# Performance work log

Hardware: AMD Instinct MI355X
Metric: run time of the kernel (lower is better)

The kernel has to match this reference:

```python
import jax, jax.numpy as jnp
import numpy as np

N_NODES = 50000
N_EDGES = 800000
IN_DIM = 128
HID = 128
NUM_CLASSES = 2


def setup_inputs() -> dict:
    key = jax.random.key(0)
    ks = jax.random.split(key, 16)
    inp = {
        "adj_row": jax.random.randint(ks[0], (N_EDGES,), 0, N_NODES),
        "adj_col": jax.random.randint(ks[1], (N_EDGES,), 0, N_NODES),
        "adj_vals": jax.random.uniform(ks[2], (N_EDGES,), dtype=jnp.float32),
        "input_feature": jax.random.normal(ks[3], (N_NODES, IN_DIM), dtype=jnp.float32),
        "graph_indicator": jax.random.randint(ks[4], (N_NODES,), 0, 64),
        # GCN layer params (kaiming-uniform-ish init; zeros bias like the torch module)
        "W1": jax.random.uniform(ks[5], (IN_DIM, HID), jnp.float32, -1, 1) * np.sqrt(6.0 / IN_DIM),
        "b1": jnp.zeros((HID,), jnp.float32),
        "W2": jax.random.uniform(ks[6], (HID, HID), jnp.float32, -1, 1) * np.sqrt(6.0 / HID),
        "b2": jnp.zeros((HID,), jnp.float32),
        "W3": jax.random.uniform(ks[7], (HID, HID), jnp.float32, -1, 1) * np.sqrt(6.0 / HID),
        "b3": jnp.zeros((HID,), jnp.float32),
        # fc params (torch.nn.Linear default init range)
        "fcW1": jax.random.uniform(ks[8], (3 * HID, HID), jnp.float32, -1, 1) / np.sqrt(3 * HID),
        "fcb1": jax.random.uniform(ks[9], (HID,), jnp.float32, -1, 1) / np.sqrt(3 * HID),
        "fcW2": jax.random.uniform(ks[10], (HID, HID // 2), jnp.float32, -1, 1) / np.sqrt(HID),
        "fcb2": jax.random.uniform(ks[11], (HID // 2,), jnp.float32, -1, 1) / np.sqrt(HID),
        "fcW3": jax.random.uniform(ks[12], (HID // 2, NUM_CLASSES), jnp.float32, -1, 1) / np.sqrt(HID // 2),
        "fcb3": jax.random.uniform(ks[13], (NUM_CLASSES,), jnp.float32, -1, 1) / np.sqrt(HID // 2),
    }
    return inp


def _gcn_layer(row, col, vals, x, W, b, n_nodes):
    # support = X @ W  -> dense GEMM
    support = x @ W
    # sparse.mm(A, support): out[i] = sum_{e: row[e]=i} vals[e] * support[col[e]]
    msgs = support[col] * vals[:, None]  # [E, D] gather + scale
    agg = jax.ops.segment_sum(msgs, row, num_segments=n_nodes)
    return agg + b


def reference(adj_row, adj_col, adj_vals, input_feature, graph_indicator,
              W1, b1, W2, b2, W3, b3, fcW1, fcb1, fcW2, fcb2, fcW3, fcb3):
    n = input_feature.shape[0]
    g1 = jax.nn.relu(_gcn_layer(adj_row, adj_col, adj_vals, input_feature, W1, b1, n))
    g2 = jax.nn.relu(_gcn_layer(adj_row, adj_col, adj_vals, g1, W2, b2, n))
    g3 = jax.nn.relu(_gcn_layer(adj_row, adj_col, adj_vals, g2, W3, b3, n))
    feat = jnp.concatenate([g1, g2, g3], axis=1)  # [N, 3*HID]
    h = jax.nn.relu(feat @ fcW1 + fcb1)
    h = jax.nn.relu(h @ fcW2 + fcb2)
    logits = h @ fcW3 + fcb3
    return logits
```

## Files before the change

kernel.cpp:

```cpp
#include <hip/hip_runtime.h>
#include <hip/hip_bf16.h>

#define N_NODES 50000
#define N_EDGES 800000
#define NBK 391
#define BCAP 2560
#define PADSLACK 896

static inline int cdiv(int a, int b) { return (a + b - 1) / b; }

typedef __attribute__((ext_vector_type(8))) short short8;
typedef __attribute__((ext_vector_type(4))) float f32x4;

__device__ __forceinline__ float b2f(unsigned short u) {
    union { unsigned int i; float f; } c;
    c.i = ((unsigned int)u) << 16;
    return c.f;
}
__device__ __forceinline__ unsigned short f2bb(float f) {
    __hip_bfloat16 h = __float2bfloat16(f);
    return *(unsigned short*)&h;
}

__device__ __forceinline__ void pack_one(const float* __restrict__ W,
                                         __hip_bfloat16* __restrict__ out,
                                         int K, int N, int t) {
    int lane = t & 63;
    int kc = (t >> 6) % (K / 32);
    int nt = (t >> 6) / (K / 32);
    int kbase = kc * 32 + (lane >> 4) * 8;
    int col = nt * 16 + (lane & 15);
    __hip_bfloat16* dst = out + (size_t)t * 8;
#pragma unroll
    for (int j = 0; j < 8; ++j)
        dst[j] = __float2bfloat16(W[(size_t)(kbase + j) * N + col]);
}

__global__ __launch_bounds__(256)
void stage1_kernel(const int* __restrict__ row, const int* __restrict__ col,
                   const float* __restrict__ vals, int* __restrict__ bcursor,
                   int2* __restrict__ tmp, int E,
                   const float* __restrict__ x, __hip_bfloat16* __restrict__ support,
                   int M,
                   const float* __restrict__ W1, const float* __restrict__ W2,
                   const float* __restrict__ W3, const float* __restrict__ fcW1,
                   const float* __restrict__ fcW2,
                   __hip_bfloat16* __restrict__ pW2, __hip_bfloat16* __restrict__ pW3,
                   __hip_bfloat16* __restrict__ pfcW1, __hip_bfloat16* __restrict__ pfcW2) {
    __shared__ unsigned short As[64][136];
    __shared__ int hist[NBK];
    __shared__ int base[NBK];
    const int b = blockIdx.x;
    const int tid = threadIdx.x;

    if (b < 196) {
        const int CH = 4096;
        int e0 = b * CH;
        for (int i = tid; i < NBK; i += 256) hist[i] = 0;
        __syncthreads();
        for (int i = tid; i < CH; i += 256) {
            int e = e0 + i;
            if (e < E) atomicAdd(&hist[row[e] >> 7], 1);
        }
        __syncthreads();
        for (int i = tid; i < NBK; i += 256) {
            int c = hist[i];
            base[i] = (c > 0) ? (i * BCAP + atomicAdd(&bcursor[i], c)) : 0;
            hist[i] = 0;
        }
        __syncthreads();
        for (int i = tid; i < CH; i += 256) {
            int e = e0 + i;
            if (e < E) {
                int r = row[e];
                int bk = r >> 7;
                int rk = atomicAdd(&hist[bk], 1);
                tmp[base[bk] + rk] = make_int2(((r & 127) << 16) | col[e],
                                               __float_as_int(vals[e]));
            }
        }
        return;
    }

    if (b < 978) {
        const int wave = tid >> 6;
        const int lane = tid & 63;
        const int ln15 = lane & 15;
        const int quad = lane >> 4;
        const int m0 = (b - 196) * 64;

        short8 bfr[4][2];
#pragma unroll
        for (int kc = 0; kc < 4; ++kc)
#pragma unroll
            for (int h = 0; h < 2; ++h)
#pragma unroll
                for (int j = 0; j < 8; ++j)
                    bfr[kc][h][j] = (short)f2bb(
                        W1[(size_t)(kc * 32 + quad * 8 + j) * 128 + (wave * 2 + h) * 16 + ln15]);

#pragma unroll
        for (int i = 0; i < 4; ++i) {
            int idx = tid + i * 256;
            int r = idx >> 4;
            int c8 = (idx & 15) * 8;
            uint4 pk = {0, 0, 0, 0};
            if (m0 + r < M) {
                const float* src = &x[(size_t)(m0 + r) * 128 + c8];
                float4 a = *(const float4*)src;
                float4 bq = *(const float4*)(src + 4);
                pk.x = f2bb(a.x) | ((unsigned int)f2bb(a.y) << 16);
                pk.y = f2bb(a.z) | ((unsigned int)f2bb(a.w) << 16);
                pk.z = f2bb(bq.x) | ((unsigned int)f2bb(bq.y) << 16);
                pk.w = f2bb(bq.z) | ((unsigned int)f2bb(bq.w) << 16);
            }
            *(uint4*)&As[r][c8] = pk;
        }
        __syncthreads();

        f32x4 acc[4][2];
#pragma unroll
        for (int s = 0; s < 4; ++s)
#pragma unroll
            for (int h = 0; h < 2; ++h) acc[s][h] = (f32x4){0.f, 0.f, 0.f, 0.f};
#pragma unroll
        for (int kc = 0; kc < 4; ++kc) {
            short8 af[4];
#pragma unroll
            for (int s = 0; s < 4; ++s)
                af[s] = *(const short8*)&As[s * 16 + ln15][kc * 32 + quad * 8];
#pragma unroll
            for (int s = 0; s < 4; ++s)
#pragma unroll
                for (int h = 0; h < 2; ++h)
                    acc[s][h] = __builtin_amdgcn_mfma_f32_16x16x32_bf16(
                        af[s], bfr[kc][h], acc[s][h], 0, 0, 0);
        }
#pragma unroll
        for (int s = 0; s < 4; ++s)
#pragma unroll
            for (int h = 0; h < 2; ++h) {
                int cl = (wave * 2 + h) * 16 + ln15;
#pragma unroll
                for (int r = 0; r < 4; ++r) {
                    int rw = m0 + s * 16 + quad * 4 + r;
                    if (rw < M)
                        support[(size_t)rw * 128 + cl] = __float2bfloat16(acc[s][h][r]);
                }
            }
        return;
    }

    int pb = b - 978;
    if (pb < 8)       pack_one(W2,  pW2,  128, 128, pb * 256 + tid);
    else if (pb < 16) pack_one(W3,  pW3,  128, 128, (pb - 8) * 256 + tid);
    else if (pb < 40) pack_one(fcW1, pfcW1, 384, 128, (pb - 16) * 256 + tid);
    else              pack_one(fcW2, pfcW2, 128, 64, (pb - 40) * 256 + tid);
}


__global__ __launch_bounds__(512)
void bscan_kernel(const int* __restrict__ bcursor, int* __restrict__ bbase) {
    __shared__ int s[512];
    int t = threadIdx.x;
    int v = (t < NBK) ? bcursor[t] : 0;
    s[t] = v;
    __syncthreads();
    for (int off = 1; off < 512; off <<= 1) {
        int u = (t >= off) ? s[t - off] : 0;
        __syncthreads();
        s[t] += u;
        __syncthreads();
    }
    if (t < NBK) bbase[t] = s[t] - v;
    if (t == NBK - 1) bbase[NBK] = s[t];
}

__global__ __launch_bounds__(256)
void binB_kernel(const int2* __restrict__ tmp, const int* __restrict__ bcursor,
                 const int* __restrict__ bbase, int* __restrict__ row_ptr,
                 int* __restrict__ row_end, int2* __restrict__ epack, int N) {
    int b = blockIdx.x;
    int r0 = b << 7;
    int nr = N - r0; if (nr > 128) nr = 128;
    __shared__ int cnt[128];
    __shared__ int cur[128];
    __shared__ int rpos[128];
    int t = threadIdx.x;
    if (t < 128) cnt[t] = 0;
    __syncthreads();
    int slab = b * BCAP;
    int send = slab + bcursor[b];
    for (int i = slab + t; i < send; i += 256)
        atomicAdd(&cnt[tmp[i].x >> 16], 1);
    __syncthreads();
    int rcnt = (t < 128) ? cnt[t] : 0;
    int pc = (rcnt + 7) & ~7;
    if (t < 128) cur[t] = pc;
    __syncthreads();
    for (int off = 1; off < 128; off <<= 1) {
        int u = (t >= off && t < 128) ? cur[t - off] : 0;
        __syncthreads();
        if (t < 128) cur[t] += u;
        __syncthreads();
    }
    int obase = bbase[b] + b * PADSLACK;
    if (t < 128) {
        int pos = obase + cur[t] - pc;
        rpos[t] = pos;
        cur[t] = pos;
        if (t < nr) {
            row_ptr[r0 + t] = pos;
            row_end[r0 + t] = pos + pc;
        }
    }
    __syncthreads();
    for (int i = slab + t; i < send; i += 256) {
        int2 v = tmp[i];
        int rl = v.x >> 16;
        int c = v.x & 0xffff;
        int pos = atomicAdd(&cur[rl], 1);
        epack[pos] = make_int2(c, v.y);
    }
    if (t < 128) {
        int pos = rpos[t];
#pragma unroll 1
        for (int i = pos + rcnt; i < pos + pc; ++i)
            epack[i] = make_int2(0, 0);
    }
}

__global__ __launch_bounds__(256, 3)
void mfma_gemm(const __hip_bfloat16* __restrict__ A, int lda,
               const __hip_bfloat16* __restrict__ pW,
               __hip_bfloat16* __restrict__ C, int M) {
    __shared__ unsigned short As[64][136];
    const int tid = threadIdx.x;
    const int wave = tid >> 6;
    const int lane = tid & 63;
    const int ln15 = lane & 15;
    const int quad = lane >> 4;
    const int m0 = blockIdx.x * 64;
    const int ntw = wave * 2;

    f32x4 acc[4][2];
#pragma unroll
    for (int s = 0; s < 4; ++s)
#pragma unroll
        for (int h = 0; h < 2; ++h) acc[s][h] = (f32x4){0.f, 0.f, 0.f, 0.f};

#pragma unroll
    for (int i = 0; i < 4; ++i) {
        int idx = tid + i * 256;
        int r = idx >> 4;
        int c8 = (idx & 15) * 8;
        uint4 v = *(const uint4*)&A[(size_t)(m0 + r) * lda + c8];
        *(uint4*)&As[r][c8] = v;
    }
    __syncthreads();
#pragma unroll
    for (int kc = 0; kc < 4; ++kc) {
        short8 af[4];
#pragma unroll
        for (int s = 0; s < 4; ++s)
            af[s] = *(const short8*)&As[s * 16 + ln15][kc * 32 + quad * 8];
        short8 bf[2];
#pragma unroll
        for (int h = 0; h < 2; ++h)
            bf[h] = *(const short8*)&pW[((size_t)((ntw + h) * 4 + kc) * 64 + lane) * 8];
#pragma unroll
        for (int s = 0; s < 4; ++s)
#pragma unroll
            for (int h = 0; h < 2; ++h)
                acc[s][h] = __builtin_amdgcn_mfma_f32_16x16x32_bf16(
                    af[s], bf[h], acc[s][h], 0, 0, 0);
    }

#pragma unroll
    for (int s = 0; s < 4; ++s)
#pragma unroll
        for (int h = 0; h < 2; ++h) {
            int cl = (ntw + h) * 16 + ln15;
#pragma unroll
            for (int r = 0; r < 4; ++r) {
                int rw = m0 + s * 16 + quad * 4 + r;
                if (rw < M)
                    C[(size_t)rw * 128 + cl] = __float2bfloat16(acc[s][h][r]);
            }
        }
}

__global__ __launch_bounds__(256)
void spmm_kernel(const int* __restrict__ row_ptr, const int* __restrict__ row_end,
                 const int2* __restrict__ epack,
                 const __hip_bfloat16* __restrict__ support,
                 const float* __restrict__ bias, __hip_bfloat16* __restrict__ out,
                 int ldo, int n) {
    int wv = threadIdx.x >> 6;
    int l = threadIdx.x & 63;
    int node = blockIdx.x * 4 + wv;
    if (node >= n) return;
    const long long* ep = (const long long*)epack;
    int p = row_ptr[node], end = row_end[node];
    float ax = 0.f, ay = 0.f;
    long long v[8];
    ushort2 u[8];
    bool have = false;
    if (p < end) {
#pragma unroll
        for (int j = 0; j < 8; ++j) v[j] = ep[p + j];
#pragma unroll
        for (int j = 0; j < 8; ++j)
            u[j] = *(const ushort2*)&support[(size_t)(unsigned int)(v[j] & 0xffffffffu) * 128 + l * 2];
        p += 8;
        have = true;
    }
    while (p < end) {
        long long v2[8];
        ushort2 u2[8];
#pragma unroll
        for (int j = 0; j < 8; ++j) v2[j] = ep[p + j];
#pragma unroll
        for (int j = 0; j < 8; ++j)
            u2[j] = *(const ushort2*)&support[(size_t)(unsigned int)(v2[j] & 0xffffffffu) * 128 + l * 2];
#pragma unroll
        for (int j = 0; j < 8; ++j) {
            float f = __int_as_float((int)(v[j] >> 32));
            ax += f * b2f(u[j].x);
            ay += f * b2f(u[j].y);
        }
#pragma unroll
        for (int j = 0; j < 8; ++j) { v[j] = v2[j]; u[j] = u2[j]; }
        p += 8;
    }
    if (have) {
#pragma unroll
        for (int j = 0; j < 8; ++j) {
            float f = __int_as_float((int)(v[j] >> 32));
            ax += f * b2f(u[j].x);
            ay += f * b2f(u[j].y);
        }
    }
    unsigned int packed = (unsigned int)f2bb(fmaxf(ax + bias[l * 2 + 0], 0.f))
                        | ((unsigned int)f2bb(fmaxf(ay + bias[l * 2 + 1], 0.f)) << 16);
    __builtin_nontemporal_store(packed, (unsigned int*)&out[(size_t)node * ldo + l * 2]);
}

__global__ __launch_bounds__(256, 3)
void fc123_kernel(const __hip_bfloat16* __restrict__ featb,
                  const __hip_bfloat16* __restrict__ pfcW1,
                  const float* __restrict__ fcb1,
                  const __hip_bfloat16* __restrict__ pfcW2,
                  const float* __restrict__ fcb2,
                  const float* __restrict__ fcW3, const float* __restrict__ fcb3,
                  float* __restrict__ out, int M) {
    __shared__ unsigned short As[64][136];
    __shared__ float w3s[128];
    __shared__ float b3s[2];
    const int tid = threadIdx.x;
    const int wave = tid >> 6;
    const int lane = tid & 63;
    const int ln15 = lane & 15;
    const int quad = lane >> 4;
    const int m0 = blockIdx.x * 64;
    if (tid < 128) w3s[tid] = fcW3[tid];
    if (tid < 2) b3s[tid] = fcb3[tid];

    f32x4 acc[4][2];
#pragma unroll
    for (int s = 0; s < 4; ++s)
#pragma unroll
        for (int h = 0; h < 2; ++h) acc[s][h] = (f32x4){0.f, 0.f, 0.f, 0.f};
    for (int kb = 0; kb < 3; ++kb) {
#pragma unroll
        for (int i = 0; i < 4; ++i) {
            int idx = tid + i * 256;
            int r = idx >> 4;
            int c8 = (idx & 15) * 8;
            uint4 v = *(const uint4*)&featb[(size_t)(m0 + r) * 384 + kb * 128 + c8];
            *(uint4*)&As[r][c8] = v;
        }
        __syncthreads();
#pragma unroll
        for (int kc = 0; kc < 4; ++kc) {
            short8 af[4];
#pragma unroll
            for (int s = 0; s < 4; ++s)
                af[s] = *(const short8*)&As[s * 16 + ln15][kc * 32 + quad * 8];
            short8 bf[2];
#pragma unroll
            for (int h = 0; h < 2; ++h) {
                int kcg = kb * 4 + kc;
                bf[h] = *(const short8*)&pfcW1[((size_t)((wave * 2 + h) * 12 + kcg) * 64 + lane) * 8];
            }
#pragma unroll
            for (int s = 0; s < 4; ++s)
#pragma unroll
                for (int h = 0; h < 2; ++h)
                    acc[s][h] = __builtin_amdgcn_mfma_f32_16x16x32_bf16(
                        af[s], bf[h], acc[s][h], 0, 0, 0);
        }
        __syncthreads();
    }
#pragma unroll
    for (int s = 0; s < 4; ++s)
#pragma unroll
        for (int h = 0; h < 2; ++h) {
            int col = (wave * 2 + h) * 16 + ln15;
            float bv = fcb1[col];
#pragma unroll
            for (int r = 0; r < 4; ++r) {
                int row = s * 16 + quad * 4 + r;
                As[row][col] = f2bb(fmaxf(acc[s][h][r] + bv, 0.f));
            }
        }
    __syncthreads();

    f32x4 acc2[4];
#pragma unroll
    for (int s = 0; s < 4; ++s) acc2[s] = (f32x4){0.f, 0.f, 0.f, 0.f};
#pragma unroll
    for (int kc = 0; kc < 4; ++kc) {
        short8 af[4];
#pragma unroll
        for (int s = 0; s < 4; ++s)
            af[s] = *(const short8*)&As[s * 16 + ln15][kc * 32 + quad * 8];
        short8 bfw = *(const short8*)&pfcW2[((size_t)(wave * 4 + kc) * 64 + lane) * 8];
#pragma unroll
        for (int s = 0; s < 4; ++s)
            acc2[s] = __builtin_amdgcn_mfma_f32_16x16x32_bf16(af[s], bfw, acc2[s], 0, 0, 0);
    }
    __syncthreads();
    {
        int col2 = wave * 16 + ln15;
        float bv = fcb2[col2];
#pragma unroll
        for (int s = 0; s < 4; ++s)
#pragma unroll
            for (int r = 0; r < 4; ++r) {
                int row = s * 16 + quad * 4 + r;
                As[row][col2] = f2bb(fmaxf(acc2[s][r] + bv, 0.f));
            }
    }
    __syncthreads();

    if (tid < 128) {
        int row = tid >> 1, cls = tid & 1;
        int grow = m0 + row;
        if (grow < M) {
            float a = b3s[cls];
#pragma unroll
            for (int k = 0; k < 64; ++k)
                a += b2f(As[row][k]) * w3s[k * 2 + cls];
            out[(size_t)grow * 2 + cls] = a;
        }
    }
}

extern "C" void kernel_launch(void* const* d_in, const int* in_sizes, int n_in,
                              void* d_out, int out_size, void* d_ws, size_t ws_size,
                              hipStream_t stream) {
    const int*   adj_row  = (const int*)d_in[0];
    const int*   adj_col  = (const int*)d_in[1];
    const float* adj_vals = (const float*)d_in[2];
    const float* x        = (const float*)d_in[3];
    const float* W1   = (const float*)d_in[5];
    const float* b1   = (const float*)d_in[6];
    const float* W2   = (const float*)d_in[7];
    const float* b2   = (const float*)d_in[8];
    const float* W3   = (const float*)d_in[9];
    const float* b3   = (const float*)d_in[10];
    const float* fcW1 = (const float*)d_in[11];
    const float* fcb1 = (const float*)d_in[12];
    const float* fcW2 = (const float*)d_in[13];
    const float* fcb2 = (const float*)d_in[14];
    const float* fcW3 = (const float*)d_in[15];
    const float* fcb3 = (const float*)d_in[16];
    float* out = (float*)d_out;

    const int N = N_NODES, E = N_EDGES;
    const int Mpad = 50048;
    const int EPAD = E + NBK * PADSLACK + 64;

    char* p = (char*)d_ws;
    auto alloc = [&](size_t bytes) {
        char* q = p;
        p += (bytes + 255) & ~(size_t)255;
        return q;
    };
    __hip_bfloat16* featb    = (__hip_bfloat16*)alloc((size_t)Mpad * 384 * 2);
    __hip_bfloat16* supportb = (__hip_bfloat16*)alloc((size_t)Mpad * 128 * 2);
    __hip_bfloat16* pW2   = (__hip_bfloat16*)alloc(16384 * 2);
    __hip_bfloat16* pW3   = (__hip_bfloat16*)alloc(16384 * 2);
    __hip_bfloat16* pfcW1 = (__hip_bfloat16*)alloc(49152 * 2);
    __hip_bfloat16* pfcW2 = (__hip_bfloat16*)alloc(8192 * 2);
    int*   row_ptr   = (int*)alloc((size_t)(N + 1) * 4);
    int*   row_end   = (int*)alloc((size_t)(N + 1) * 4);
    int*   bbase     = (int*)alloc((size_t)(NBK + 1) * 4);
    int*   bcursor   = (int*)alloc((size_t)NBK * 4);
    int2*  epack     = (int2*)alloc((size_t)EPAD * 8);
    int2*  tmp       = (int2*)alloc((size_t)NBK * BCAP * 8);

    hipMemsetAsync(bcursor, 0, (size_t)NBK * 4, stream);
    stage1_kernel<<<1022, 256, 0, stream>>>(adj_row, adj_col, adj_vals, bcursor, tmp, E,
                                            x, supportb, N,
                                            W1, W2, W3, fcW1, fcW2,
                                            pW2, pW3, pfcW1, pfcW2);
    bscan_kernel<<<1, 512, 0, stream>>>(bcursor, bbase);
    binB_kernel<<<NBK, 256, 0, stream>>>(tmp, bcursor, bbase, row_ptr, row_end, epack, N);

    const int gemmGrid = cdiv(N, 64);
    const int spmmGrid = cdiv(N, 4);

    spmm_kernel<<<spmmGrid, 256, 0, stream>>>(row_ptr, row_end, epack, supportb, b1,
                                              featb + 0, 384, N);
    mfma_gemm<<<gemmGrid, 256, 0, stream>>>(featb + 0, 384, pW2, supportb, N);
    spmm_kernel<<<spmmGrid, 256, 0, stream>>>(row_ptr, row_end, epack, supportb, b2,
                                              featb + 128, 384, N);
    mfma_gemm<<<gemmGrid, 256, 0, stream>>>(featb + 128, 384, pW3, supportb, N);
    spmm_kernel<<<spmmGrid, 256, 0, stream>>>(row_ptr, row_end, epack, supportb, b3,
                                              featb + 256, 384, N);

    fc123_kernel<<<gemmGrid, 256, 0, stream>>>(featb, pfcW1, fcb1, pfcW2, fcb2,
                                               fcW3, fcb3, out, N);
}
```

Before: 280.7 us.

## Vectorize SpMM gathers to 16-byte loads and fold bucket scan into binning

The SpMM kernel now splits each wave into four 16-lane groups. Each group gathers a full 256-byte support row with uint4 loads, covering eight edges per iteration, and the partial sums are reduced across groups with shuffles. This replaces eight narrow 4-byte gathers per lane. The separate single-block bucket-scan kernel is removed: each binB block now computes its own prefix sum over bcursor with a block reduction. Row start and end are packed into one int2 array, which adds redundant prefix work per block in exchange for one fewer launch and fewer scattered loads.

```diff
diff --git a/kernel.cpp b/kernel.cpp
--- a/kernel.cpp
+++ b/kernel.cpp
@@ -159,36 +159,26 @@
 }
 
 
-__global__ __launch_bounds__(512)
-void bscan_kernel(const int* __restrict__ bcursor, int* __restrict__ bbase) {
-    __shared__ int s[512];
-    int t = threadIdx.x;
-    int v = (t < NBK) ? bcursor[t] : 0;
-    s[t] = v;
-    __syncthreads();
-    for (int off = 1; off < 512; off <<= 1) {
-        int u = (t >= off) ? s[t - off] : 0;
-        __syncthreads();
-        s[t] += u;
-        __syncthreads();
-    }
-    if (t < NBK) bbase[t] = s[t] - v;
-    if (t == NBK - 1) bbase[NBK] = s[t];
-}
-
 __global__ __launch_bounds__(256)
 void binB_kernel(const int2* __restrict__ tmp, const int* __restrict__ bcursor,
-                 const int* __restrict__ bbase, int* __restrict__ row_ptr,
-                 int* __restrict__ row_end, int2* __restrict__ epack, int N) {
+                 int2* __restrict__ rowrange, int2* __restrict__ epack, int N) {
     int b = blockIdx.x;
     int r0 = b << 7;
     int nr = N - r0; if (nr > 128) nr = 128;
     __shared__ int cnt[128];
     __shared__ int cur[128];
     __shared__ int rpos[128];
+    __shared__ int red[256];
     int t = threadIdx.x;
+    int partial = 0;
+    for (int i = t; i < b; i += 256) partial += bcursor[i];
+    red[t] = partial;
     if (t < 128) cnt[t] = 0;
     __syncthreads();
+    for (int off = 128; off > 0; off >>= 1) {
+        if (t < off) red[t] += red[t + off];
+        __syncthreads();
+    }
     int slab = b * BCAP;
     int send = slab + bcursor[b];
     for (int i = slab + t; i < send; i += 256)
@@ -204,15 +194,12 @@
         if (t < 128) cur[t] += u;
         __syncthreads();
     }
-    int obase = bbase[b] + b * PADSLACK;
+    int obase = red[0] + b * PADSLACK;
     if (t < 128) {
         int pos = obase + cur[t] - pc;
         rpos[t] = pos;
         cur[t] = pos;
-        if (t < nr) {
-            row_ptr[r0 + t] = pos;
-            row_end[r0 + t] = pos + pc;
-        }
+        if (t < nr) rowrange[r0 + t] = make_int2(pos, pos + pc);
     }
     __syncthreads();
     for (int i = slab + t; i < send; i += 256) {
@@ -223,9 +210,10 @@
         epack[pos] = make_int2(c, v.y);
     }
     if (t < 128) {
+        int rc = rcnt;
         int pos = rpos[t];
 #pragma unroll 1
-        for (int i = pos + rcnt; i < pos + pc; ++i)
+        for (int i = pos + rc; i < pos + pc; ++i)
             epack[i] = make_int2(0, 0);
     }
 }
@@ -290,8 +278,20 @@
         }
 }
 
+__device__ __forceinline__ void accum8(float* acc, long long e, uint4 u) {
+    float f = __int_as_float((int)(e >> 32));
+    acc[0] += f * b2f((unsigned short)(u.x & 0xffff));
+    acc[1] += f * b2f((unsigned short)(u.x >> 16));
+    acc[2] += f * b2f((unsigned short)(u.y & 0xffff));
+    acc[3] += f * b2f((unsigned short)(u.y >> 16));
+    acc[4] += f * b2f((unsigned short)(u.z & 0xffff));
+    acc[5] += f * b2f((unsigned short)(u.z >> 16));
+    acc[6] += f * b2f((unsigned short)(u.w & 0xffff));
+    acc[7] += f * b2f((unsigned short)(u.w >> 16));
+}
+
 __global__ __launch_bounds__(256)
-void spmm_kernel(const int* __restrict__ row_ptr, const int* __restrict__ row_end,
+void spmm_kernel(const int2* __restrict__ rowrange,
                  const int2* __restrict__ epack,
                  const __hip_bfloat16* __restrict__ support,
                  const float* __restrict__ bias, __hip_bfloat16* __restrict__ out,
@@ -300,50 +300,60 @@
     int l = threadIdx.x & 63;
     int node = blockIdx.x * 4 + wv;
     if (node >= n) return;
+    const int g = l >> 4;
+    const int j = l & 15;
     const long long* ep = (const long long*)epack;
-    int p = row_ptr[node], end = row_end[node];
-    float ax = 0.f, ay = 0.f;
-    long long v[8];
-    ushort2 u[8];
+    int2 rr = rowrange[node];
+    int p = rr.x, end = rr.y;
+
+    float acc[8];
+#pragma unroll
+    for (int k = 0; k < 8; ++k) acc[k] = 0.f;
+
+    long long e0 = 0, e1 = 0;
+    uint4 u0 = {0, 0, 0, 0}, u1 = {0, 0, 0, 0};
     bool have = false;
     if (p < end) {
-#pragma unroll
-        for (int j = 0; j < 8; ++j) v[j] = ep[p + j];
-#pragma unroll
-        for (int j = 0; j < 8; ++j)
-            u[j] = *(const ushort2*)&support[(size_t)(unsigned int)(v[j] & 0xffffffffu) * 128 + l * 2];
+        e0 = ep[p + g];
+        e1 = ep[p + 4 + g];
+        u0 = *(const uint4*)&support[(size_t)(unsigned int)(e0 & 0xffffffffu) * 128 + j * 8];
+        u1 = *(const uint4*)&support[(size_t)(unsigned int)(e1 & 0xffffffffu) * 128 + j * 8];
         p += 8;
         have = true;
     }
     while (p < end) {
-        long long v2[8];
-        ushort2 u2[8];
-#pragma unroll
-        for (int j = 0; j < 8; ++j) v2[j] = ep[p + j];
-#pragma unroll
-        for (int j = 0; j < 8; ++j)
-            u2[j] = *(const ushort2*)&support[(size_t)(unsigned int)(v2[j] & 0xffffffffu) * 128 + l * 2];
-#pragma unroll
-        for (int j = 0; j < 8; ++j) {
-            float f = __int_as_float((int)(v[j] >> 32));
-            ax += f * b2f(u[j].x);
-            ay += f * b2f(u[j].y);
-        }
-#pragma unroll
-        for (int j = 0; j < 8; ++j) { v[j] = v2[j]; u[j] = u2[j]; }
+        long long f0 = ep[p + g];
+        long long f1 = ep[p + 4 + g];
+        uint4 w0 = *(const uint4*)&support[(size_t)(unsigned int)(f0 & 0xffffffffu) * 128 + j * 8];
+        uint4 w1 = *(const uint4*)&support[(size_t)(unsigned int)(f1 & 0xffffffffu) * 128 + j * 8];
+        accum8(acc, e0, u0);
+        accum8(acc, e1, u1);
+        e0 = f0; u0 = w0; e1 = f1; u1 = w1;
         p += 8;
     }
     if (have) {
-#pragma unroll
-        for (int j = 0; j < 8; ++j) {
-            float f = __int_as_float((int)(v[j] >> 32));
-            ax += f * b2f(u[j].x);
-            ay += f * b2f(u[j].y);
-        }
-    }
-    unsigned int packed = (unsigned int)f2bb(fmaxf(ax + bias[l * 2 + 0], 0.f))
-                        | ((unsigned int)f2bb(fmaxf(ay + bias[l * 2 + 1], 0.f)) << 16);
-    __builtin_nontemporal_store(packed, (unsigned int*)&out[(size_t)node * ldo + l * 2]);
+        accum8(acc, e0, u0);
+        accum8(acc, e1, u1);
+    }
+#pragma unroll
+    for (int k = 0; k < 8; ++k) {
+        acc[k] += __shfl_xor(acc[k], 16);
+        acc[k] += __shfl_xor(acc[k], 32);
+    }
+    if (g == 0) {
+        float4 b0 = *(const float4*)&bias[j * 8];
+        float4 b1 = *(const float4*)&bias[j * 8 + 4];
+        unsigned int q0 = (unsigned int)f2bb(fmaxf(acc[0] + b0.x, 0.f))
+                        | ((unsigned int)f2bb(fmaxf(acc[1] + b0.y, 0.f)) << 16);
+        unsigned int q1 = (unsigned int)f2bb(fmaxf(acc[2] + b0.z, 0.f))
+                        | ((unsigned int)f2bb(fmaxf(acc[3] + b0.w, 0.f)) << 16);
+        unsigned int q2 = (unsigned int)f2bb(fmaxf(acc[4] + b1.x, 0.f))
+                        | ((unsigned int)f2bb(fmaxf(acc[5] + b1.y, 0.f)) << 16);
+        unsigned int q3 = (unsigned int)f2bb(fmaxf(acc[6] + b1.z, 0.f))
+                        | ((unsigned int)f2bb(fmaxf(acc[7] + b1.w, 0.f)) << 16);
+        uint4 st = {q0, q1, q2, q3};
+        *(uint4*)&out[(size_t)node * ldo + j * 8] = st;
+    }
 }
 
 __global__ __launch_bounds__(256, 3)
@@ -494,9 +504,7 @@
     __hip_bfloat16* pW3   = (__hip_bfloat16*)alloc(16384 * 2);
     __hip_bfloat16* pfcW1 = (__hip_bfloat16*)alloc(49152 * 2);
     __hip_bfloat16* pfcW2 = (__hip_bfloat16*)alloc(8192 * 2);
-    int*   row_ptr   = (int*)alloc((size_t)(N + 1) * 4);
-    int*   row_end   = (int*)alloc((size_t)(N + 1) * 4);
-    int*   bbase     = (int*)alloc((size_t)(NBK + 1) * 4);
+    int2*  rowrange  = (int2*)alloc((size_t)(N + 1) * 8);
     int*   bcursor   = (int*)alloc((size_t)NBK * 4);
     int2*  epack     = (int2*)alloc((size_t)EPAD * 8);
     int2*  tmp       = (int2*)alloc((size_t)NBK * BCAP * 8);
@@ -506,19 +514,18 @@
                                             x, supportb, N,
                                             W1, W2, W3, fcW1, fcW2,
                                             pW2, pW3, pfcW1, pfcW2);
-    bscan_kernel<<<1, 512, 0, stream>>>(bcursor, bbase);
-    binB_kernel<<<NBK, 256, 0, stream>>>(tmp, bcursor, bbase, row_ptr, row_end, epack, N);
+    binB_kernel<<<NBK, 256, 0, stream>>>(tmp, bcursor, rowrange, epack, N);
 
     const int gemmGrid = cdiv(N, 64);
     const int spmmGrid = cdiv(N, 4);
 
-    spmm_kernel<<<spmmGrid, 256, 0, stream>>>(row_ptr, row_end, epack, supportb, b1,
+    spmm_kernel<<<spmmGrid, 256, 0, stream>>>(rowrange, epack, supportb, b1,
                                               featb + 0, 384, N);
     mfma_gemm<<<gemmGrid, 256, 0, stream>>>(featb + 0, 384, pW2, supportb, N);
-    spmm_kernel<<<spmmGrid, 256, 0, stream>>>(row_ptr, row_end, epack, supportb, b2,
+    spmm_kernel<<<spmmGrid, 256, 0, stream>>>(rowrange, epack, supportb, b2,
                                               featb + 128, 384, N);
     mfma_gemm<<<gemmGrid, 256, 0, stream>>>(featb + 128, 384, pW3, supportb, N);
-    spmm_kernel<<<spmmGrid, 256, 0, stream>>>(row_ptr, row_end, epack, supportb, b3,
+    spmm_kernel<<<spmmGrid, 256, 0, stream>>>(rowrange, epack, supportb, b3,
                                               featb + 256, 384, N);
 
     fc123_kernel<<<gemmGrid, 256, 0, stream>>>(featb, pfcW1, fcb1, pfcW2, fcb2,
```

Measured after the change: 268.0 us. 4.5% less time.
